# Optimization experiments

Measured on AMD Instinct MI355X. Metric: run time of the kernel, lower is better.

The kernel has to match this reference:

```python
import jax, jax.numpy as jnp
import numpy as np

B, M, D = 8, 1024, 1024
H = 16
HD = D // H  # 64
F = 4096

def layer_norm(x, gamma, beta, eps=1e-5):
    mu = jnp.mean(x, axis=-1, keepdims=True)
    var = jnp.var(x, axis=-1, keepdims=True)
    return (x - mu) * jax.lax.rsqrt(var + eps) * gamma + beta

def setup_inputs() -> dict:
    key = jax.random.key(0)
    ks = jax.random.split(key, 16)
    s = 0.02
    return {
        "h": jax.random.normal(ks[0], (B, M, D), jnp.float32),
        "h_all": jax.random.normal(ks[1], (B, M, D), jnp.float32),
        "Wq": jax.random.normal(ks[2], (D, D), jnp.float32) * s,
        "Wk": jax.random.normal(ks[3], (D, D), jnp.float32) * s,
        "Wv": jax.random.normal(ks[4], (D, D), jnp.float32) * s,
        "Wo": jax.random.normal(ks[5], (D, D), jnp.float32) * s,
        "W1": jax.random.normal(ks[6], (D, F), jnp.float32) * s,
        "b1": jnp.zeros((F,), jnp.float32),
        "W2": jax.random.normal(ks[7], (F, D), jnp.float32) * s,
        "b2": jnp.zeros((D,), jnp.float32),
        "g1": jnp.ones((D,), jnp.float32),
        "be1": jnp.zeros((D,), jnp.float32),
        "g2": jnp.ones((D,), jnp.float32),
        "be2": jnp.zeros((D,), jnp.float32),
    }

def reference(h, h_all, Wq, Wk, Wv, Wo, W1, b1, W2, b2, g1, be1, g2, be2):
    Bx, Mx, Dx = h.shape
    # projections (no bias, per nn.Linear(bias=False))
    q = (h @ Wq).reshape(Bx, Mx, H, HD)        # [B,M,H,hd]
    k = (h_all @ Wk).reshape(Bx, -1, H, HD)    # [B,N,H,hd]
    v = (h_all @ Wv).reshape(Bx, -1, H, HD)
    # attention: scale by sqrt(head_dim) as in SeqAttention(hidden_size=head_dim)
    scores = jnp.einsum('bqhd,bkhd->bhqk', q, k) / jnp.sqrt(jnp.float32(HD))
    attn = jax.nn.softmax(scores, axis=-1)
    ctx = jnp.einsum('bhqk,bkhd->bqhd', attn, v).reshape(Bx, Mx, Dx)
    attn_out = ctx @ Wo
    # post-norm residual 1
    h1 = layer_norm(h + attn_out, g1, be1)
    # FFN
    ff = jax.nn.relu(h1 @ W1 + b1) @ W2 + b2
    # post-norm residual 2
    out = layer_norm(h1 + ff, g2, be2)
    return out
```

## Files before the change

kernel.cpp:

```cpp
#include <hip/hip_runtime.h>
#include <hip/hip_bf16.h>

#define ROWS 8192
#define DD   1024
#define HH   16
#define HD   64
#define FF   4096

typedef __attribute__((ext_vector_type(4))) float f32x4;
typedef __attribute__((ext_vector_type(8))) __bf16 bf16x8;

static __device__ __forceinline__ unsigned short f2bf(float f) {
  unsigned u = __float_as_uint(f);
  u += 0x7fffu + ((u >> 16) & 1u);
  return (unsigned short)(u >> 16);
}

static __device__ __forceinline__ f32x4 mfma16(bf16x8 a, bf16x8 b, f32x4 c) {
  return __builtin_amdgcn_mfma_f32_16x16x32_bf16(a, b, c, 0, 0, 0);
}

#define GLOAD16(gp, lp) __builtin_amdgcn_global_load_lds( \
    (__attribute__((address_space(1))) void*)(gp), \
    (__attribute__((address_space(3))) void*)(lp), 16, 0, 0)

__global__ __launch_bounds__(256) void cast_bf16_k(
    const float* __restrict__ in, unsigned short* __restrict__ out, int n4) {
  int i = blockIdx.x * 256 + threadIdx.x;
  if (i >= n4) return;
  float4 v = ((const float4*)in)[i];
  ushort4 o;
  o.x = f2bf(v.x); o.y = f2bf(v.y); o.z = f2bf(v.z); o.w = f2bf(v.w);
  ((ushort4*)out)[i] = o;
}

__global__ __launch_bounds__(256) void transpose_cast_k(
    const float* __restrict__ in, unsigned short* __restrict__ out, int R, int C) {
  __shared__ float tile[32][33];
  int bx = blockIdx.x * 32;
  int by = blockIdx.y * 32;
  int tx = threadIdx.x, ty = threadIdx.y;
  #pragma unroll
  for (int i = 0; i < 32; i += 8)
    tile[ty + i][tx] = in[(size_t)(by + ty + i) * C + bx + tx];
  __syncthreads();
  #pragma unroll
  for (int i = 0; i < 32; i += 8)
    out[(size_t)(bx + ty + i) * R + by + tx] = f2bf(tile[tx][ty + i]);
}

template <int BM, int MODE>
__global__ __launch_bounds__(512, 2) void gemm256(
    const unsigned short* __restrict__ A, const unsigned short* __restrict__ BT,
    const float* __restrict__ bias, void* __restrict__ Cout, void* __restrict__ Cout2,
    int Ni, int Ki, int nbx) {
  constexpr int LA = BM / 64;
  constexpr int MR = BM / 32;
  __shared__ unsigned short As[2][BM * 64];
  __shared__ unsigned short Bs[2][256 * 64];

  const int tid  = threadIdx.x;
  const int lane = tid & 63;
  const int wid  = tid >> 6;
  const int wm   = wid >> 2;
  const int wn   = wid & 3;
  const int lr   = lane & 15;
  const int kq   = lane >> 4;
  const int axor = (lr & 7) << 4;

  const int nwg = gridDim.x;
  const int cpx = nwg >> 3;
  const int wg  = (int)blockIdx.x;
  const int swz = (wg & 7) * cpx + (wg >> 3);
  const int bx = swz % nbx, by = swz / nbx;
  const int brow = by * BM, bcol = bx * 256;

  const int srow = wid * 8 + (lane >> 3);
  const int scol = ((lane & 7) * 8) ^ ((srow & 7) << 3);
  size_t offA[LA], offB[4];
  #pragma unroll
  for (int L = 0; L < LA; ++L)
    offA[L] = (size_t)(brow + L * 64 + srow) * Ki + scol;
  #pragma unroll
  for (int L = 0; L < 4; ++L)
    offB[L] = (size_t)(bcol + L * 64 + srow) * Ki + scol;

  auto stage = [&](int t, int d) {
    #pragma unroll
    for (int L = 0; L < LA; ++L)
      GLOAD16(A + offA[L] + t * 64, (char*)As[d] + L * 8192 + wid * 1024);
    #pragma unroll
    for (int L = 0; L < 4; ++L)
      GLOAD16(BT + offB[L] + t * 64, (char*)Bs[d] + L * 8192 + wid * 1024);
  };

  f32x4 acc[MR][4] = {};
  const int NT = Ki >> 6;

  stage(0, 0);
  stage(1, 1);

  #pragma unroll 1
  for (int t = 0; t < NT; ++t) {
    const int d = t & 1;
    if constexpr (BM == 256) asm volatile("s_waitcnt vmcnt(8)" ::: "memory");
    else                     asm volatile("s_waitcnt vmcnt(6)" ::: "memory");
    __builtin_amdgcn_s_barrier();
    __builtin_amdgcn_sched_barrier(0);

    const unsigned short* as = As[d];
    const unsigned short* bs = Bs[d];
    #pragma unroll
    for (int kk = 0; kk < 2; ++kk) {
      bf16x8 af[MR], bfv[4];
      #pragma unroll
      for (int m = 0; m < MR; ++m)
        af[m] = *(const bf16x8*)((const char*)as +
            (wm * (BM / 2) + m * 16 + lr) * 128 + ((kk * 64 + kq * 16) ^ axor));
      #pragma unroll
      for (int n = 0; n < 4; ++n)
        bfv[n] = *(const bf16x8*)((const char*)bs +
            (wn * 64 + n * 16 + lr) * 128 + ((kk * 64 + kq * 16) ^ axor));
      #pragma unroll
      for (int m = 0; m < MR; ++m)
        #pragma unroll
        for (int n = 0; n < 4; ++n)
          acc[m][n] = mfma16(af[m], bfv[n], acc[m][n]);
    }

    asm volatile("s_waitcnt lgkmcnt(0)" ::: "memory");
    __builtin_amdgcn_s_barrier();
    __builtin_amdgcn_sched_barrier(0);
    const int ts = (t + 2 < NT) ? t + 2 : NT - 1;
    stage(ts, d);
  }

  #pragma unroll
  for (int m = 0; m < MR; ++m) {
    #pragma unroll
    for (int n = 0; n < 4; ++n) {
      const int r0 = brow + wm * (BM / 2) + m * 16 + kq * 4;
      const int c  = bcol + wn * 64 + n * 16 + lr;
      if constexpr (MODE == 4) {
        if (c < 1024) {
          #pragma unroll
          for (int e = 0; e < 4; ++e)
            ((unsigned short*)Cout)[(size_t)(r0 + e) * 1024 + c] = f2bf(acc[m][n][e]);
        } else {
          const int cc = c - 1024;
          const int bq = r0 >> 10;
          const int tok = r0 & 1023;
          ushort4 pk;
          pk.x = f2bf(acc[m][n][0]); pk.y = f2bf(acc[m][n][1]);
          pk.z = f2bf(acc[m][n][2]); pk.w = f2bf(acc[m][n][3]);
          *(ushort4*)((unsigned short*)Cout2 + ((size_t)bq * 1024 + cc) * 1024 + tok) = pk;
        }
      } else {
        const float bv = (MODE == 2 || MODE == 3) ? bias[c] : 0.0f;
        #pragma unroll
        for (int e = 0; e < 4; ++e) {
          float v = acc[m][n][e] + bv;
          if (MODE == 2) v = fmaxf(v, 0.0f);
          if (MODE == 0 || MODE == 2)
            ((unsigned short*)Cout)[(size_t)(r0 + e) * Ni + c] = f2bf(v);
          else
            ((float*)Cout)[(size_t)(r0 + e) * Ni + c] = v;
        }
      }
    }
  }
}

__global__ __launch_bounds__(512, 4) void attn_k(
    const unsigned short* __restrict__ q, const unsigned short* __restrict__ k,
    const unsigned short* __restrict__ vT, unsigned short* __restrict__ ctx) {
  __shared__ unsigned short Ks[2][64 * 64];
  __shared__ unsigned short Vt[2][64 * 64];
  __shared__ unsigned short Ps[8][16 * 64];
  const int tid = threadIdx.x;
  const int lane = tid & 63;
  const int wid = tid >> 6;
  const int bh = blockIdx.y;
  const int b = bh >> 4, h = bh & 15;
  const int qrow0 = blockIdx.x * 128 + wid * 16;
  const size_t tokbase = (size_t)b * 1024;
  const int lr = lane & 15, kq = lane >> 4;

  const int srow = tid >> 3;
  const int scol = ((tid & 7) * 8) ^ ((srow & 7) << 3);
  const unsigned short* kg = k + (tokbase + srow) * 1024 + h * 64 + scol;
  const unsigned short* vg = vT + ((size_t)(b * 16 + h) * 64 + srow) * 1024 + scol;
  const int ldst = tid * 16;

  auto stage = [&](int kt, int d) {
    GLOAD16(kg + (size_t)kt * 64 * 1024, (char*)Ks[d] + ldst);
    GLOAD16(vg + kt * 64, (char*)Vt[d] + ldst);
  };

  bf16x8 aq[2];
  {
    const unsigned short* qp = q + (tokbase + qrow0 + lr) * DD + h * 64 + kq * 8;
    aq[0] = *(const bf16x8*)qp;
    aq[1] = *(const bf16x8*)(qp + 32);
  }

  float l_part[4] = {0.f, 0.f, 0.f, 0.f};
  f32x4 acc[4] = {};
  const float C = 0.125f * 1.4426950408889634f;

  stage(0, 0);
  stage(1, 1);

  #pragma unroll 2
  for (int kt = 0; kt < 16; ++kt) {
    const int d = kt & 1;
    asm volatile("s_waitcnt vmcnt(2)" ::: "memory");
    __builtin_amdgcn_s_barrier();
    __builtin_amdgcn_sched_barrier(0);

    f32x4 sv[4] = {};
    #pragma unroll
    for (int jb = 0; jb < 4; ++jb)
      #pragma unroll
      for (int ks = 0; ks < 2; ++ks) {
        int row = jb * 16 + lr;
        bf16x8 bk = *(const bf16x8*)((const char*)Ks[d] +
            row * 128 + ((ks * 64 + kq * 16) ^ ((row & 7) << 4)));
        sv[jb] = mfma16(aq[ks], bk, sv[jb]);
      }

    #pragma unroll
    for (int jb = 0; jb < 4; ++jb)
      #pragma unroll
      for (int j = 0; j < 4; ++j) {
        float p = exp2f(sv[jb][j] * C);
        sv[jb][j] = p;
        l_part[j] += p;
      }

    #pragma unroll
    for (int jb = 0; jb < 4; ++jb)
      #pragma unroll
      for (int j = 0; j < 4; ++j) {
        int row = kq * 4 + j;
        *(unsigned short*)((char*)Ps[wid] +
            ((row * 128 + (jb * 16 + lr) * 2) ^ ((row & 7) << 4))) = f2bf(sv[jb][j]);
      }

    #pragma unroll
    for (int ks = 0; ks < 2; ++ks) {
      bf16x8 ap = *(const bf16x8*)((const char*)Ps[wid] +
          lr * 128 + ((ks * 64 + kq * 16) ^ ((lr & 7) << 4)));
      #pragma unroll
      for (int db = 0; db < 4; ++db) {
        int dd = db * 16 + lr;
        bf16x8 bv = *(const bf16x8*)((const char*)Vt[d] +
            dd * 128 + ((ks * 64 + kq * 16) ^ ((dd & 7) << 4)));
        acc[db] = mfma16(ap, bv, acc[db]);
      }
    }

    asm volatile("s_waitcnt lgkmcnt(0)" ::: "memory");
    __builtin_amdgcn_s_barrier();
    __builtin_amdgcn_sched_barrier(0);
    const int ts = (kt + 2 < 16) ? kt + 2 : 15;
    stage(ts, d);
  }

  #pragma unroll
  for (int j = 0; j < 4; ++j) {
    float l = l_part[j];
    #pragma unroll
    for (int mk = 1; mk < 16; mk <<= 1) l += __shfl_xor(l, mk);
    float inv = 1.0f / l;
    int r = qrow0 + kq * 4 + j;
    #pragma unroll
    for (int db = 0; db < 4; ++db)
      ctx[(tokbase + r) * DD + h * 64 + db * 16 + lr] = f2bf(acc[db][j] * inv);
  }
}

template <int WB>
__global__ __launch_bounds__(256) void ln_add_k(
    const float* __restrict__ a, const float* __restrict__ b,
    const float* __restrict__ gamma, const float* __restrict__ beta,
    float* __restrict__ outf, unsigned short* __restrict__ outb) {
  int row = blockIdx.x;
  int tid = threadIdx.x;
  size_t base = (size_t)row * 1024 + tid * 4;
  float4 va = *(const float4*)(a + base);
  float4 vb = *(const float4*)(b + base);
  float x[4] = {va.x + vb.x, va.y + vb.y, va.z + vb.z, va.w + vb.w};
  float s = x[0] + x[1] + x[2] + x[3];
  float sq = x[0] * x[0] + x[1] * x[1] + x[2] * x[2] + x[3] * x[3];
  #pragma unroll
  for (int mk = 1; mk < 64; mk <<= 1) {
    s += __shfl_xor(s, mk);
    sq += __shfl_xor(sq, mk);
  }
  __shared__ float red[8];
  int wid = tid >> 6, lane = tid & 63;
  if (lane == 0) { red[wid] = s; red[4 + wid] = sq; }
  __syncthreads();
  s = red[0] + red[1] + red[2] + red[3];
  sq = red[4] + red[5] + red[6] + red[7];
  float mu = s * (1.0f / 1024.0f);
  float var = sq * (1.0f / 1024.0f) - mu * mu;
  float rs = rsqrtf(var + 1e-5f);
  float4 g = *(const float4*)(gamma + tid * 4);
  float4 be = *(const float4*)(beta + tid * 4);
  float y[4];
  y[0] = (x[0] - mu) * rs * g.x + be.x;
  y[1] = (x[1] - mu) * rs * g.y + be.y;
  y[2] = (x[2] - mu) * rs * g.z + be.z;
  y[3] = (x[3] - mu) * rs * g.w + be.w;
  float4 o; o.x = y[0]; o.y = y[1]; o.z = y[2]; o.w = y[3];
  *(float4*)(outf + base) = o;
  if (WB) {
    ushort4 ob;
    ob.x = f2bf(y[0]); ob.y = f2bf(y[1]); ob.z = f2bf(y[2]); ob.w = f2bf(y[3]);
    *(ushort4*)(outb + base) = ob;
  }
}

extern "C" void kernel_launch(void* const* d_in, const int* in_sizes, int n_in,
                              void* d_out, int out_size, void* d_ws, size_t ws_size,
                              hipStream_t stream) {
  const float* h    = (const float*)d_in[0];
  const float* hall = (const float*)d_in[1];
  const float* Wq   = (const float*)d_in[2];
  const float* Wk   = (const float*)d_in[3];
  const float* Wv   = (const float*)d_in[4];
  const float* Wo   = (const float*)d_in[5];
  const float* W1   = (const float*)d_in[6];
  const float* b1   = (const float*)d_in[7];
  const float* W2   = (const float*)d_in[8];
  const float* b2   = (const float*)d_in[9];
  const float* g1   = (const float*)d_in[10];
  const float* be1  = (const float*)d_in[11];
  const float* g2   = (const float*)d_in[12];
  const float* be2  = (const float*)d_in[13];

  char* ws = (char*)d_ws;
  size_t off = 0;
  auto alloc = [&](size_t n) { size_t o = off; off += (n + 255) & ~(size_t)255; return o; };
  const size_t hb_o   = alloc((size_t)ROWS * DD * 2);
  const size_t hab_o  = alloc((size_t)ROWS * DD * 2);
  const size_t wqt_o  = alloc((size_t)DD * DD * 2);
  const size_t wkvt_o = alloc((size_t)DD * DD * 4);
  const size_t wot_o  = alloc((size_t)DD * DD * 2);
  const size_t w1t_o  = alloc((size_t)DD * FF * 2);
  const size_t w2t_o  = alloc((size_t)FF * DD * 2);
  const size_t qb_o   = alloc((size_t)ROWS * DD * 2);
  const size_t kb_o   = alloc((size_t)ROWS * DD * 2);
  const size_t vt_o   = alloc((size_t)ROWS * DD * 2);
  const size_t cx_o   = alloc((size_t)ROWS * DD * 2);
  const size_t h1_o   = alloc((size_t)ROWS * DD * 4);
  const size_t h1b_o  = alloc((size_t)ROWS * DD * 2);

  unsigned short* hb   = (unsigned short*)(ws + hb_o);
  unsigned short* hab  = (unsigned short*)(ws + hab_o);
  unsigned short* wqt  = (unsigned short*)(ws + wqt_o);
  unsigned short* wkvt = (unsigned short*)(ws + wkvt_o);
  unsigned short* wot  = (unsigned short*)(ws + wot_o);
  unsigned short* w1t  = (unsigned short*)(ws + w1t_o);
  unsigned short* w2t  = (unsigned short*)(ws + w2t_o);
  unsigned short* qb   = (unsigned short*)(ws + qb_o);
  unsigned short* kb   = (unsigned short*)(ws + kb_o);
  unsigned short* vTb  = (unsigned short*)(ws + vt_o);
  unsigned short* cxb  = (unsigned short*)(ws + cx_o);
  float*          h1   = (float*)(ws + h1_o);
  unsigned short* h1b  = (unsigned short*)(ws + h1b_o);
  float*          attn_out = (float*)(ws + hb_o);
  unsigned short* ff1      = (unsigned short*)(ws + qb_o);
  float*          outf     = (float*)d_out;

  cast_bf16_k<<<ROWS * DD / 1024, 256, 0, stream>>>(h, hb, ROWS * DD / 4);
  cast_bf16_k<<<ROWS * DD / 1024, 256, 0, stream>>>(hall, hab, ROWS * DD / 4);
  dim3 tb(32, 8);
  transpose_cast_k<<<dim3(32, 32), tb, 0, stream>>>(Wq, wqt, DD, DD);
  transpose_cast_k<<<dim3(32, 32), tb, 0, stream>>>(Wk, wkvt, DD, DD);
  transpose_cast_k<<<dim3(32, 32), tb, 0, stream>>>(Wv, wkvt + (size_t)DD * DD, DD, DD);
  transpose_cast_k<<<dim3(32, 32), tb, 0, stream>>>(Wo, wot, DD, DD);
  transpose_cast_k<<<dim3(128, 32), tb, 0, stream>>>(W1, w1t, DD, FF);
  transpose_cast_k<<<dim3(32, 128), tb, 0, stream>>>(W2, w2t, FF, DD);

  gemm256<128, 0><<<dim3(256), 512, 0, stream>>>(hb,  wqt,  nullptr, qb, nullptr, DD,   DD, 4);
  gemm256<256, 4><<<dim3(256), 512, 0, stream>>>(hab, wkvt, nullptr, kb, vTb,    2048, DD, 8);

  attn_k<<<dim3(8, 128), 512, 0, stream>>>(qb, kb, vTb, cxb);

  gemm256<128, 1><<<dim3(256), 512, 0, stream>>>(cxb, wot, nullptr, attn_out, nullptr, DD, DD, 4);
  ln_add_k<1><<<ROWS, 256, 0, stream>>>(h, attn_out, g1, be1, h1, h1b);

  gemm256<256, 2><<<dim3(512), 512, 0, stream>>>(h1b, w1t, b1, ff1, nullptr, FF, DD, 16);
  gemm256<128, 3><<<dim3(256), 512, 0, stream>>>(ff1, w2t, b2, outf, nullptr, DD, FF, 4);

  ln_add_k<0><<<ROWS, 256, 0, stream>>>(h1, outf, g2, be2, outf, nullptr);
}
```

Baseline: 398.8 us.

## Split-K the FFN down-projection and fold partial sums into final layernorm

The W2 GEMM changes from 256 tiles of 128x256 over the full K=4096 to BM=256 tiles split into two K halves. Each half writes its own fp32 partial, with the bias added only by the first. A new three-input layernorm kernel sums h1 and both partials before normalising, so no atomic or separate reduction kernel is needed. The attention kernel's launch bounds are also raised to 6 waves per SIMD for occupancy, which may force register spills. The split-K path adds an extra 32 MB fp32 partial write and read in exchange for larger tiles with better reuse.

```diff
diff --git a/kernel.cpp b/kernel.cpp
--- a/kernel.cpp
+++ b/kernel.cpp
@@ -49,7 +49,7 @@
     out[(size_t)(bx + ty + i) * R + by + tx] = f2bf(tile[tx][ty + i]);
 }
 
-template <int BM, int MODE>
+template <int BM, int MODE, int KS = 1>
 __global__ __launch_bounds__(512, 2) void gemm256(
     const unsigned short* __restrict__ A, const unsigned short* __restrict__ BT,
     const float* __restrict__ bias, void* __restrict__ Cout, void* __restrict__ Cout2,
@@ -72,18 +72,23 @@
   const int cpx = nwg >> 3;
   const int wg  = (int)blockIdx.x;
   const int swz = (wg & 7) * cpx + (wg >> 3);
-  const int bx = swz % nbx, by = swz / nbx;
+  const int perk = nwg / KS;
+  const int kh   = swz / perk;
+  const int swzr = swz % perk;
+  const int bx = swzr % nbx, by = swzr / nbx;
   const int brow = by * BM, bcol = bx * 256;
+  const int Kc   = Ki / KS;
+  const int kbase = kh * Kc;
 
   const int srow = wid * 8 + (lane >> 3);
   const int scol = ((lane & 7) * 8) ^ ((srow & 7) << 3);
   size_t offA[LA], offB[4];
   #pragma unroll
   for (int L = 0; L < LA; ++L)
-    offA[L] = (size_t)(brow + L * 64 + srow) * Ki + scol;
+    offA[L] = (size_t)(brow + L * 64 + srow) * Ki + kbase + scol;
   #pragma unroll
   for (int L = 0; L < 4; ++L)
-    offB[L] = (size_t)(bcol + L * 64 + srow) * Ki + scol;
+    offB[L] = (size_t)(bcol + L * 64 + srow) * Ki + kbase + scol;
 
   auto stage = [&](int t, int d) {
     #pragma unroll
@@ -95,7 +100,7 @@
   };
 
   f32x4 acc[MR][4] = {};
-  const int NT = Ki >> 6;
+  const int NT = Kc >> 6;
 
   stage(0, 0);
   stage(1, 1);
@@ -155,6 +160,12 @@
           pk.z = f2bf(acc[m][n][2]); pk.w = f2bf(acc[m][n][3]);
           *(ushort4*)((unsigned short*)Cout2 + ((size_t)bq * 1024 + cc) * 1024 + tok) = pk;
         }
+      } else if constexpr (MODE == 5) {
+        float* o = (kh == 0) ? (float*)Cout : (float*)Cout2;
+        const float bv = (kh == 0) ? bias[c] : 0.0f;
+        #pragma unroll
+        for (int e = 0; e < 4; ++e)
+          o[(size_t)(r0 + e) * Ni + c] = acc[m][n][e] + bv;
       } else {
         const float bv = (MODE == 2 || MODE == 3) ? bias[c] : 0.0f;
         #pragma unroll
@@ -171,7 +182,7 @@
   }
 }
 
-__global__ __launch_bounds__(512, 4) void attn_k(
+__global__ __launch_bounds__(512, 6) void attn_k(
     const unsigned short* __restrict__ q, const unsigned short* __restrict__ k,
     const unsigned short* __restrict__ vT, unsigned short* __restrict__ ctx) {
   __shared__ unsigned short Ks[2][64 * 64];
@@ -323,6 +334,45 @@
   }
 }
 
+__global__ __launch_bounds__(256) void ln3_k(
+    const float* __restrict__ a, const float* __restrict__ b,
+    const float* __restrict__ c,
+    const float* __restrict__ gamma, const float* __restrict__ beta,
+    float* __restrict__ outf) {
+  int row = blockIdx.x;
+  int tid = threadIdx.x;
+  size_t base = (size_t)row * 1024 + tid * 4;
+  float4 va = *(const float4*)(a + base);
+  float4 vb = *(const float4*)(b + base);
+  float4 vc = *(const float4*)(c + base);
+  float x[4] = {va.x + vb.x + vc.x, va.y + vb.y + vc.y,
+                va.z + vb.z + vc.z, va.w + vb.w + vc.w};
+  float s = x[0] + x[1] + x[2] + x[3];
+  float sq = x[0] * x[0] + x[1] * x[1] + x[2] * x[2] + x[3] * x[3];
+  #pragma unroll
+  for (int mk = 1; mk < 64; mk <<= 1) {
+    s += __shfl_xor(s, mk);
+    sq += __shfl_xor(sq, mk);
+  }
+  __shared__ float red[8];
+  int wid = tid >> 6, lane = tid & 63;
+  if (lane == 0) { red[wid] = s; red[4 + wid] = sq; }
+  __syncthreads();
+  s = red[0] + red[1] + red[2] + red[3];
+  sq = red[4] + red[5] + red[6] + red[7];
+  float mu = s * (1.0f / 1024.0f);
+  float var = sq * (1.0f / 1024.0f) - mu * mu;
+  float rs = rsqrtf(var + 1e-5f);
+  float4 g = *(const float4*)(gamma + tid * 4);
+  float4 be = *(const float4*)(beta + tid * 4);
+  float4 o;
+  o.x = (x[0] - mu) * rs * g.x + be.x;
+  o.y = (x[1] - mu) * rs * g.y + be.y;
+  o.z = (x[2] - mu) * rs * g.z + be.z;
+  o.w = (x[3] - mu) * rs * g.w + be.w;
+  *(float4*)(outf + base) = o;
+}
+
 extern "C" void kernel_launch(void* const* d_in, const int* in_sizes, int n_in,
                               void* d_out, int out_size, void* d_ws, size_t ws_size,
                               hipStream_t stream) {
@@ -372,6 +422,7 @@
   float*          h1   = (float*)(ws + h1_o);
   unsigned short* h1b  = (unsigned short*)(ws + h1b_o);
   float*          attn_out = (float*)(ws + hb_o);
+  float*          ff2p1    = (float*)(ws + hb_o);
   unsigned short* ff1      = (unsigned short*)(ws + qb_o);
   float*          outf     = (float*)d_out;
 
@@ -393,8 +444,8 @@
   gemm256<128, 1><<<dim3(256), 512, 0, stream>>>(cxb, wot, nullptr, attn_out, nullptr, DD, DD, 4);
   ln_add_k<1><<<ROWS, 256, 0, stream>>>(h, attn_out, g1, be1, h1, h1b);
 
-  gemm256<256, 2><<<dim3(512), 512, 0, stream>>>(h1b, w1t, b1, ff1, nullptr, FF, DD, 16);
-  gemm256<128, 3><<<dim3(256), 512, 0, stream>>>(ff1, w2t, b2, outf, nullptr, DD, FF, 4);
-
-  ln_add_k<0><<<ROWS, 256, 0, stream>>>(h1, outf, g2, be2, outf, nullptr);
-}
+  gemm256<256, 2>   <<<dim3(512), 512, 0, stream>>>(h1b, w1t, b1, ff1, nullptr, FF, DD, 16);
+  gemm256<256, 5, 2><<<dim3(256), 512, 0, stream>>>(ff1, w2t, b2, outf, ff2p1, DD, FF, 4);
+
+  ln3_k<<<ROWS, 256, 0, stream>>>(h1, outf, ff2p1, g2, be2, outf);
+}
```

Measured after the change: 391.2 us. Within noise of the previous version (-1.9%).
